# Kernel optimization log

Measured on AMD Instinct MI355X. Metric: run time of the kernel, lower is better.

The kernel has to match this reference:

```python
import jax, jax.numpy as jnp
import numpy as np


def setup_inputs() -> dict:
    key = jax.random.key(0)
    ks = jax.random.split(key, 6)
    bs, n_src, n_tgt = 4, 4096, 16384
    c_src, c_tgt = 256, 128
    xyz_target = jax.random.uniform(ks[0], (bs, n_tgt, 3), dtype=jnp.float32)
    xyz_source = jax.random.uniform(ks[1], (bs, n_src, 3), dtype=jnp.float32)
    feats_target = jax.random.normal(ks[2], (bs, n_tgt, c_tgt), dtype=jnp.float32)
    feats_source = jax.random.normal(ks[3], (bs, n_src, c_src), dtype=jnp.float32)
    # SharedMlP 1x1 conv weights (1,1,cin,cout) squeezed to (cin,cout)
    w1 = jax.random.normal(ks[4], (c_src + c_tgt, 256), dtype=jnp.float32) * (1.0 / np.sqrt(c_src + c_tgt))
    w2 = jax.random.normal(ks[5], (256, 256), dtype=jnp.float32) * (1.0 / np.sqrt(256))
    return {"xyz_target": xyz_target, "xyz_source": xyz_source,
            "feats_target": feats_target, "feats_source": feats_source,
            "w1": w1, "w2": w2}


def reference(xyz_target, xyz_source, feats_target, feats_source, w1, w2):
    # --- three_nn: full pairwise euclidean distance [bs, n_tgt, n_src] ---
    diff = xyz_target[:, :, None, :] - xyz_source[:, None, :, :]
    dis = jnp.linalg.norm(diff, axis=-1)                      # bs, n_tgt, n_src
    neg_dis, idx = jax.lax.top_k(-dis, 3)                     # 3 nearest
    nn_dis = jnp.maximum(-neg_dis, 1e-10)                     # bs, n_tgt, 3
    inv = 1.0 / nn_dis
    weight = inv / jnp.sum(inv, axis=-1, keepdims=True)       # bs, n_tgt, 3
    # --- three_interpolate: batched gather + weighted reduce ---
    feats_sel = jax.vmap(lambda f, i: f[i])(feats_source, idx)  # bs, n_tgt, 3, c
    w_sum = jnp.sum(weight, axis=-1, keepdims=True) + 1e-6
    interp = jnp.einsum('btk,btkc->btc', weight, feats_sel) / w_sum
    # --- concat skip features, 1x1-conv MLP (pointwise matmul) ---
    x = jnp.concatenate([interp, feats_target], axis=2)       # bs, n_tgt, 384
    x = jax.nn.relu(jnp.einsum('btc,cd->btd', x, w1))
    x = jax.nn.relu(jnp.einsum('btc,cd->btd', x, w2))
    return x
```

## Files before the change

### kernel.cpp

```cpp
#include <hip/hip_runtime.h>
#include <hip/hip_bf16.h>
#include <stdint.h>

#define BS 4
#define NS 4096
#define NT 16384
#define CT 128
#define NOUT 256
#define MTOT (BS*NT)
#define GR 8
#define NC (GR*GR*GR)
#define HCELL 0.125f

typedef __attribute__((ext_vector_type(4))) float floatx4;
typedef __attribute__((ext_vector_type(8))) unsigned short ushortx8;
typedef __attribute__((ext_vector_type(8))) __bf16 bf16x8;

__device__ __forceinline__ unsigned short f2bf(float f) {
  unsigned int u = __builtin_bit_cast(unsigned int, f);
  u += 0x7FFFu + ((u >> 16) & 1u);
  return (unsigned short)(u >> 16);
}
__device__ __forceinline__ float bf2f(unsigned short u) {
  return __builtin_bit_cast(float, ((unsigned int)u) << 16);
}
__device__ __forceinline__ int cell_of(float x) {
  int c = (int)(x * 8.0f);
  return min(7, max(0, c));
}
__device__ __forceinline__ bf16x8 ldb16(const unsigned short* p) {
  return __builtin_bit_cast(bf16x8, *(const ushortx8*)p);
}
__device__ __forceinline__ ushortx8 wsum8(ushortx8 a, ushortx8 c, ushortx8 e,
                                          float w0, float w1v, float w2v) {
  ushortx8 o;
  #pragma unroll
  for (int q = 0; q < 8; ++q)
    o[q] = f2bf(w0*bf2f(a[q]) + w1v*bf2f(c[q]) + w2v*bf2f(e[q]));
  return o;
}

__global__ __launch_bounds__(1024) void prep_kernel(
    const float* __restrict__ xyzs, const float* __restrict__ xyzt,
    const float* __restrict__ w1, const float* __restrict__ w2,
    float4* __restrict__ bsrc, int* __restrict__ soff, float4* __restrict__ stgt,
    unsigned short* __restrict__ w1at, unsigned short* __restrict__ w1bt,
    unsigned short* __restrict__ w2t) {
  int bid = blockIdx.x, tid = threadIdx.x;
  if (bid < 8) {
    __shared__ int cnt[NC];
    __shared__ int scan[NC];
    int b = bid & 3;
    bool isrc = bid < 4;
    int per = isrc ? (NS >> 10) : (NT >> 10);
    const float* in = isrc ? xyzs + (size_t)b * NS * 3 : xyzt + (size_t)b * NT * 3;
    float4* outp = isrc ? bsrc + (size_t)b * NS : stgt + (size_t)b * NT;
    if (tid < NC) cnt[tid] = 0;
    __syncthreads();
    for (int k = 0; k < per; ++k) {
      int p = k * 1024 + tid;
      float x = in[3*p], y = in[3*p+1], z = in[3*p+2];
      int c = (cell_of(z) * GR + cell_of(y)) * GR + cell_of(x);
      atomicAdd(&cnt[c], 1);
    }
    __syncthreads();
    if (tid < NC) scan[tid] = cnt[tid];
    __syncthreads();
    for (int off = 1; off < NC; off <<= 1) {
      int v = (tid < NC && tid >= off) ? scan[tid - off] : 0;
      __syncthreads();
      if (tid < NC) scan[tid] += v;
      __syncthreads();
    }
    if (tid < NC) {
      int excl = scan[tid] - cnt[tid];
      cnt[tid] = excl;
      if (isrc) soff[b * (NC + 1) + tid] = excl;
    }
    if (isrc && tid == 0) soff[b * (NC + 1) + NC] = NS;
    __syncthreads();
    for (int k = 0; k < per; ++k) {
      int p = k * 1024 + tid;
      float x = in[3*p], y = in[3*p+1], z = in[3*p+2];
      int c = (cell_of(z) * GR + cell_of(y)) * GR + cell_of(x);
      int slot = atomicAdd(&cnt[c], 1);
      outp[slot] = make_float4(x, y, z, __int_as_float(p));
    }
  } else {
    int i = (bid - 8) * 1024 + tid;
    int n = i >> 8, k = i & 255;
    w1at[i] = f2bf(w1[k * NOUT + n]);
    w2t[i]  = f2bf(w2[k * NOUT + n]);
    if (i < 256 * 128) {
      int n2 = i >> 7, k2 = i & 127;
      w1bt[i] = f2bf(w1[(256 + k2) * NOUT + n2]);
    }
  }
}

__device__ __forceinline__ void ins3(float sc, int jj,
    float& d0, float& d1, float& d2, int& i0, int& i1, int& i2) {
  bool l0 = sc < d0, l1 = sc < d1, l2 = sc < d2;
  d2 = l1 ? d1 : (l2 ? sc : d2);
  i2 = l1 ? i1 : (l2 ? jj : i2);
  d1 = l0 ? d0 : (l1 ? sc : d1);
  i1 = l0 ? i0 : (l1 ? jj : i1);
  d0 = l0 ? sc : d0;
  i0 = l0 ? jj : i0;
}

__device__ __forceinline__ void pair_merge(float& d0, float& d1, float& d2,
                                           int& i0, int& i1, int& i2,
                                           int delta, int sub) {
  float e0 = __shfl_xor(d0, delta);
  float e1 = __shfl_xor(d1, delta);
  float e2 = __shfl_xor(d2, delta);
  int   y0 = __shfl_xor(i0, delta);
  int   y1 = __shfl_xor(i1, delta);
  int   y2 = __shfl_xor(i2, delta);
  float a0,a1,a2,b0,b1,b2; int x0,x1,x2,z0,z1,z2;
  if ((sub & delta) == 0) { a0=d0;a1=d1;a2=d2; x0=i0;x1=i1;x2=i2;
                            b0=e0;b1=e1;b2=e2; z0=y0;z1=y1;z2=y2; }
  else                    { a0=e0;a1=e1;a2=e2; x0=y0;x1=y1;x2=y2;
                            b0=d0;b1=d1;b2=d2; z0=i0;z1=i1;z2=i2; }
  bool t = a0 <= b0;
  d0 = t ? a0 : b0; i0 = t ? x0 : z0;
  float na0 = t ? a1 : a0; int nx0 = t ? x1 : x0;
  float na1 = t ? a2 : a1; int nx1 = t ? x2 : x1;
  float nb0 = t ? b0 : b1; int nz0 = t ? z0 : z1;
  float nb1 = t ? b1 : b2; int nz1 = t ? z1 : z2;
  t = na0 <= nb0;
  d1 = t ? na0 : nb0; i1 = t ? nx0 : nz0;
  float ma0 = t ? na1 : na0; int mx0 = t ? nx1 : nx0;
  float mb0 = t ? nb0 : nb1; int mz0 = t ? nz0 : nz1;
  t = ma0 <= mb0;
  d2 = t ? ma0 : mb0; i2 = t ? mx0 : mz0;
}

__global__ __launch_bounds__(256) void nn_kernel(const float4* __restrict__ stgt,
    const float4* __restrict__ bsrc, const int* __restrict__ soff,
    int* __restrict__ idx_out, float* __restrict__ w_out) {
  __shared__ float4 s_src[NS];
  __shared__ int s_off[NC + 1];
  int tid = threadIdx.x;
  int b = blockIdx.x >> 7;
  int tseg = blockIdx.x & 127;
  for (int i = tid; i < NS; i += 256) s_src[i] = bsrc[(size_t)b * NS + i];
  for (int i = tid; i < NC + 1; i += 256) s_off[i] = soff[b * (NC + 1) + i];
  __syncthreads();
  int tpair = tid >> 1, half = tid & 1;
  float4 tg = stgt[(size_t)b * NT + tseg * 128 + tpair];
  float tx = tg.x, ty = tg.y, tz = tg.z;
  int cx = cell_of(tx), cy = cell_of(ty), cz = cell_of(tz);
  int wx = min(max(cx, 1), 6) - 1;
  int wy = min(max(cy, 1), 6) - 1;
  int wz = min(max(cz, 1), 6) - 1;
  float d0 = 1e30f, d1 = 1e30f, d2 = 1e30f;
  int i0 = 0, i1 = 0, i2 = 0;
  for (int r = half; r < 9; r += 2) {
    int ez = wz + r / 3, ey = wy + r % 3;
    int rowc = (ez * GR + ey) * GR + wx;
    int lo = s_off[rowc], hi = s_off[rowc + 3];
    for (int p = lo; p < hi; ++p) {
      float4 s = s_src[p];
      float dx = tx - s.x, dy = ty - s.y, dz = tz - s.z;
      float q = dx*dx + dy*dy + dz*dz;
      ins3(q, __float_as_int(s.w), d0, d1, d2, i0, i1, i2);
    }
  }
  pair_merge(d0, d1, d2, i0, i1, i2, 1, half);
  float clx = fminf(wx > 0 ? tx - wx * HCELL : 1e30f,
                    wx + 3 < GR ? (wx + 3) * HCELL - tx : 1e30f);
  float cly = fminf(wy > 0 ? ty - wy * HCELL : 1e30f,
                    wy + 3 < GR ? (wy + 3) * HCELL - ty : 1e30f);
  float clz = fminf(wz > 0 ? tz - wz * HCELL : 1e30f,
                    wz + 3 < GR ? (wz + 3) * HCELL - tz : 1e30f);
  float cl = fminf(clx, fminf(cly, clz));
  bool bad = d2 > cl * cl;
  if (__any(bad)) {
    if (bad) {
      d0 = d1 = d2 = 1e30f; i0 = i1 = i2 = 0;
      for (int p = half; p < NS; p += 2) {
        float4 s = s_src[p];
        float dx = tx - s.x, dy = ty - s.y, dz = tz - s.z;
        float q = dx*dx + dy*dy + dz*dz;
        ins3(q, __float_as_int(s.w), d0, d1, d2, i0, i1, i2);
      }
    }
    pair_merge(d0, d1, d2, i0, i1, i2, 1, half);
  }
  if (half == 0) {
    float r0 = fmaxf(sqrtf(d0), 1e-10f);
    float r1 = fmaxf(sqrtf(d1), 1e-10f);
    float r2 = fmaxf(sqrtf(d2), 1e-10f);
    float v0 = 1.f/r0, v1 = 1.f/r1, v2 = 1.f/r2;
    float sc = 1.f / ((v0 + v1 + v2) * (1.f + 1e-6f));
    size_t o = ((size_t)b * NT + tseg * 128 + tpair) * 3;
    idx_out[o] = i0; idx_out[o+1] = i1; idx_out[o+2] = i2;
    w_out[o] = v0*sc; w_out[o+1] = v1*sc; w_out[o+2] = v2*sc;
  }
}

__global__ __launch_bounds__(256, 4) void gemm_g(const float* __restrict__ fs,
    const unsigned short* __restrict__ w1at, unsigned short* __restrict__ G) {
  constexpr int LDT = 264;
  __shared__ __attribute__((aligned(16))) unsigned short sA[32 * LDT];
  int tid = threadIdx.x;
  int m0 = blockIdx.x * 32;
  int wave = tid >> 6, lane = tid & 63;
  int wn = wave * 64;
  int fr = lane & 15, quad = lane >> 4;
  const unsigned short* wbase = w1at + (size_t)(wn + fr) * 256 + quad * 8;
  #pragma unroll
  for (int i = 0; i < 4; ++i) {
    int u = tid + 256 * i;
    int r = u >> 5, k8 = (u & 31) * 8;
    const float* src = fs + (size_t)(m0 + r) * 256 + k8;
    float4 f0 = *(const float4*)src;
    float4 f1 = *(const float4*)(src + 4);
    ushortx8 o;
    o[0]=f2bf(f0.x); o[1]=f2bf(f0.y); o[2]=f2bf(f0.z); o[3]=f2bf(f0.w);
    o[4]=f2bf(f1.x); o[5]=f2bf(f1.y); o[6]=f2bf(f1.z); o[7]=f2bf(f1.w);
    *(ushortx8*)&sA[r * LDT + k8] = o;
  }
  __syncthreads();
  floatx4 zero = {0.f, 0.f, 0.f, 0.f};
  floatx4 acc[2][4];
  #pragma unroll
  for (int i = 0; i < 2; ++i)
    #pragma unroll
    for (int j = 0; j < 4; ++j) acc[i][j] = zero;
  bf16x8 wb[3][4];
  #pragma unroll
  for (int ni = 0; ni < 4; ++ni) wb[0][ni] = ldb16(wbase + (size_t)ni*16*256 + 0*32);
  #pragma unroll
  for (int ni = 0; ni < 4; ++ni) wb[1][ni] = ldb16(wbase + (size_t)ni*16*256 + 1*32);
  __builtin_amdgcn_sched_barrier(0);
  #pragma unroll
  for (int kt = 0; kt < 8; ++kt) {
    if (kt < 6) {
      #pragma unroll
      for (int ni = 0; ni < 4; ++ni)
        wb[(kt+2)%3][ni] = ldb16(wbase + (size_t)ni*16*256 + (kt+2)*32);
    }
    __builtin_amdgcn_sched_barrier(0);
    bf16x8 af[2];
    #pragma unroll
    for (int mi = 0; mi < 2; ++mi)
      af[mi] = ldb16(&sA[(mi*16 + fr)*LDT + kt*32 + quad*8]);
    #pragma unroll
    for (int mi = 0; mi < 2; ++mi)
      #pragma unroll
      for (int ni = 0; ni < 4; ++ni)
        acc[mi][ni] = __builtin_amdgcn_mfma_f32_16x16x32_bf16(
            af[mi], wb[kt%3][ni], acc[mi][ni], 0, 0, 0);
  }
  #pragma unroll
  for (int mi = 0; mi < 2; ++mi)
    #pragma unroll
    for (int ni = 0; ni < 4; ++ni)
      #pragma unroll
      for (int r = 0; r < 4; ++r) {
        int grow = m0 + mi*16 + quad*4 + r;
        int gcol = wn + ni*16 + fr;
        G[(size_t)grow * 256 + gcol] = f2bf(acc[mi][ni][r]);
      }
}

__global__ __launch_bounds__(512, 4) void fused_mlp(const float* __restrict__ ft,
    const unsigned short* __restrict__ G, const int* __restrict__ idxb,
    const float* __restrict__ wgtb, const float4* __restrict__ stgt,
    const unsigned short* __restrict__ w1bt, const unsigned short* __restrict__ w2t,
    float* __restrict__ out) {
  constexpr int LDI = 264;
  constexpr int LDF = 136;
  __shared__ __attribute__((aligned(16))) unsigned short sI[64 * LDI];
  __shared__ __attribute__((aligned(16))) unsigned short sF[64 * LDF];
  int tid = threadIdx.x;
  int row0 = blockIdx.x * 64;
  int b = row0 >> 14;
  const float4* st = stgt + ((size_t)b << 14) + (row0 & (NT - 1));
  const float* ftb = ft + (size_t)b * NT * CT;
  float* outb = out + (size_t)b * NT * NOUT;
  int wave = tid >> 6, lane = tid & 63;
  int wn = wave * 32;
  int fr = lane & 15, quad = lane >> 4;

  int r = tid >> 3, seg = tid & 7;
  const int* ip = idxb + (size_t)(row0 + r) * 3;
  const float* wp = wgtb + (size_t)(row0 + r) * 3;
  int g0i = ip[0], g1i = ip[1], g2i = ip[2];
  float w0 = wp[0], w1v = wp[1], w2v = wp[2];
  int rA = tid >> 4;
  int rB = rA + 32;
  int orig0 = __float_as_int(st[rA].w);
  int orig1 = __float_as_int(st[rB].w);

  bf16x8 wb1[2][4];
  #pragma unroll
  for (int ni = 0; ni < 2; ++ni)
    #pragma unroll
    for (int kt = 0; kt < 4; ++kt)
      wb1[ni][kt] = ldb16(w1bt + (size_t)(wn + ni*16 + fr) * CT + kt*32 + quad*8);
  __builtin_amdgcn_sched_barrier(0);

  const unsigned short* Gb = G + ((size_t)b << 20);
  const unsigned short* g0 = Gb + ((size_t)g0i << 8) + seg * 32;
  const unsigned short* g1 = Gb + ((size_t)g1i << 8) + seg * 32;
  const unsigned short* g2 = Gb + ((size_t)g2i << 8) + seg * 32;
  ushortx8 a0 = *(const ushortx8*)(g0 + 0);
  ushortx8 a1 = *(const ushortx8*)(g0 + 8);
  ushortx8 a2 = *(const ushortx8*)(g0 + 16);
  ushortx8 a3 = *(const ushortx8*)(g0 + 24);
  ushortx8 c0 = *(const ushortx8*)(g1 + 0);
  ushortx8 c1 = *(const ushortx8*)(g1 + 8);
  ushortx8 c2 = *(const ushortx8*)(g1 + 16);
  ushortx8 c3 = *(const ushortx8*)(g1 + 24);
  ushortx8 e0 = *(const ushortx8*)(g2 + 0);
  ushortx8 e1 = *(const ushortx8*)(g2 + 8);
  ushortx8 e2 = *(const ushortx8*)(g2 + 16);
  ushortx8 e3 = *(const ushortx8*)(g2 + 24);

  int k8 = (tid & 15) * 8;
  const float* srcA = ftb + (size_t)orig0 * CT + k8;
  const float* srcB = ftb + (size_t)orig1 * CT + k8;
  float4 fa0 = *(const float4*)srcA;
  float4 fa1 = *(const float4*)(srcA + 4);
  float4 fb0 = *(const float4*)srcB;
  float4 fb1 = *(const float4*)(srcB + 4);
  __builtin_amdgcn_sched_barrier(0);

  {
    unsigned short* dst = &sI[r * LDI + seg * 32];
    *(ushortx8*)(dst + 0)  = wsum8(a0, c0, e0, w0, w1v, w2v);
    *(ushortx8*)(dst + 8)  = wsum8(a1, c1, e1, w0, w1v, w2v);
    *(ushortx8*)(dst + 16) = wsum8(a2, c2, e2, w0, w1v, w2v);
    *(ushortx8*)(dst + 24) = wsum8(a3, c3, e3, w0, w1v, w2v);
  }
  {
    ushortx8 o;
    o[0]=f2bf(fa0.x); o[1]=f2bf(fa0.y); o[2]=f2bf(fa0.z); o[3]=f2bf(fa0.w);
    o[4]=f2bf(fa1.x); o[5]=f2bf(fa1.y); o[6]=f2bf(fa1.z); o[7]=f2bf(fa1.w);
    *(ushortx8*)&sF[rA * LDF + k8] = o;
    ushortx8 p;
    p[0]=f2bf(fb0.x); p[1]=f2bf(fb0.y); p[2]=f2bf(fb0.z); p[3]=f2bf(fb0.w);
    p[4]=f2bf(fb1.x); p[5]=f2bf(fb1.y); p[6]=f2bf(fb1.z); p[7]=f2bf(fb1.w);
    *(ushortx8*)&sF[rB * LDF + k8] = p;
  }
  __syncthreads();

  floatx4 zero = {0.f, 0.f, 0.f, 0.f};
  floatx4 acc[4][2];
  #pragma unroll
  for (int i = 0; i < 4; ++i)
    #pragma unroll
    for (int j = 0; j < 2; ++j) acc[i][j] = zero;

  #pragma unroll
  for (int kt = 0; kt < 4; ++kt) {
    bf16x8 af[4];
    #pragma unroll
    for (int mi = 0; mi < 4; ++mi)
      af[mi] = ldb16(&sF[(mi*16 + fr)*LDF + kt*32 + quad*8]);
    #pragma unroll
    for (int mi = 0; mi < 4; ++mi)
      #pragma unroll
      for (int ni = 0; ni < 2; ++ni)
        acc[mi][ni] = __builtin_amdgcn_mfma_f32_16x16x32_bf16(
            af[mi], wb1[ni][kt], acc[mi][ni], 0, 0, 0);
  }

  bf16x8 wb2[2][8];
  #pragma unroll
  for (int ni = 0; ni < 2; ++ni)
    #pragma unroll
    for (int kt = 0; kt < 8; ++kt)
      wb2[ni][kt] = ldb16(w2t + (size_t)(wn + ni*16 + fr) * NOUT + kt*32 + quad*8);
  __builtin_amdgcn_sched_barrier(0);

  #pragma unroll
  for (int mi = 0; mi < 4; ++mi)
    #pragma unroll
    for (int ni = 0; ni < 2; ++ni)
      #pragma unroll
      for (int rr = 0; rr < 4; ++rr) {
        int lr = mi*16 + quad*4 + rr;
        int lc = wn + ni*16 + fr;
        float v = acc[mi][ni][rr] + bf2f(sI[lr * LDI + lc]);
        sI[lr * LDI + lc] = f2bf(fmaxf(v, 0.f));
      }
  __syncthreads();

  #pragma unroll
  for (int i = 0; i < 4; ++i)
    #pragma unroll
    for (int j = 0; j < 2; ++j) acc[i][j] = zero;
  #pragma unroll
  for (int kt = 0; kt < 8; ++kt) {
    bf16x8 af[4];
    #pragma unroll
    for (int mi = 0; mi < 4; ++mi)
      af[mi] = ldb16(&sI[(mi*16 + fr)*LDI + kt*32 + quad*8]);
    #pragma unroll
    for (int mi = 0; mi < 4; ++mi)
      #pragma unroll
      for (int ni = 0; ni < 2; ++ni)
        acc[mi][ni] = __builtin_amdgcn_mfma_f32_16x16x32_bf16(
            af[mi], wb2[ni][kt], acc[mi][ni], 0, 0, 0);
  }
  #pragma unroll
  for (int mi = 0; mi < 4; ++mi)
    #pragma unroll
    for (int rr = 0; rr < 4; ++rr) {
      int lr = mi*16 + quad*4 + rr;
      int orig = __float_as_int(st[lr].w);
      float* orow = outb + (size_t)orig * NOUT;
      #pragma unroll
      for (int ni = 0; ni < 2; ++ni)
        orow[wn + ni*16 + fr] = fmaxf(acc[mi][ni][rr], 0.f);
    }
}

extern "C" void kernel_launch(void* const* d_in, const int* in_sizes, int n_in,
                              void* d_out, int out_size, void* d_ws, size_t ws_size,
                              hipStream_t stream) {
  (void)in_sizes; (void)n_in; (void)out_size; (void)ws_size;
  const float* xyzt = (const float*)d_in[0];
  const float* xyzs = (const float*)d_in[1];
  const float* ft   = (const float*)d_in[2];
  const float* fs   = (const float*)d_in[3];
  const float* w1   = (const float*)d_in[4];
  const float* w2   = (const float*)d_in[5];

  char* p = (char*)d_ws;
  unsigned short* w1at = (unsigned short*)p; p += (size_t)256*256*2;
  unsigned short* w1bt = (unsigned short*)p; p += (size_t)256*128*2;
  unsigned short* w2t  = (unsigned short*)p; p += (size_t)256*256*2;
  int*   idxb = (int*)p;   p += (size_t)MTOT*3*4;
  float* wgtb = (float*)p; p += (size_t)MTOT*3*4;
  unsigned short* G = (unsigned short*)p; p += (size_t)BS*NS*NOUT*2;
  float4* bsrc = (float4*)p; p += (size_t)BS*NS*16;
  float4* stgt = (float4*)p; p += (size_t)BS*NT*16;
  int*    soff = (int*)p;

  hipLaunchKernelGGL(prep_kernel, dim3(8 + 64), dim3(1024), 0, stream,
                     xyzs, xyzt, w1, w2, bsrc, soff, stgt, w1at, w1bt, w2t);
  hipLaunchKernelGGL(nn_kernel, dim3(512), dim3(256), 0, stream, stgt, bsrc, soff, idxb, wgtb);
  hipLaunchKernelGGL(gemm_g, dim3(BS*NS/32), dim3(256), 0, stream, fs, w1at, G);
  hipLaunchKernelGGL(fused_mlp, dim3(MTOT/64), dim3(512), 0, stream,
                     ft, G, idxb, wgtb, stgt, w1bt, w2t, (float*)d_out);
}
```

Before: 193.0 us.

## Drop precomputed source GEMM; interpolate raw features and run full K=384 GEMM

The separate gemm_g kernel, which projected source features through the first 256 rows of w1 before the gather, is removed. fused_mlp now gathers the three fp32 source feature rows, interpolates them into shared memory, and runs a single K=384 GEMM against a combined transposed w1. The weight fragments for both GEMMs are now streamed through a triple-buffered register prefetch instead of being preloaded in full. This removes one kernel launch and the bf16 G intermediate round trip, but gathers twice the bytes per neighbour (fp32 instead of bf16) and triples the first GEMM's K-work per target point (target points outnumber source points four to one).

After: 212.2 us. +10.0%, slower.

```diff
diff --git a/kernel.cpp b/kernel.cpp
--- a/kernel.cpp
+++ b/kernel.cpp
@@ -31,21 +31,12 @@
 __device__ __forceinline__ bf16x8 ldb16(const unsigned short* p) {
   return __builtin_bit_cast(bf16x8, *(const ushortx8*)p);
 }
-__device__ __forceinline__ ushortx8 wsum8(ushortx8 a, ushortx8 c, ushortx8 e,
-                                          float w0, float w1v, float w2v) {
-  ushortx8 o;
-  #pragma unroll
-  for (int q = 0; q < 8; ++q)
-    o[q] = f2bf(w0*bf2f(a[q]) + w1v*bf2f(c[q]) + w2v*bf2f(e[q]));
-  return o;
-}
 
 __global__ __launch_bounds__(1024) void prep_kernel(
     const float* __restrict__ xyzs, const float* __restrict__ xyzt,
     const float* __restrict__ w1, const float* __restrict__ w2,
     float4* __restrict__ bsrc, int* __restrict__ soff, float4* __restrict__ stgt,
-    unsigned short* __restrict__ w1at, unsigned short* __restrict__ w1bt,
-    unsigned short* __restrict__ w2t) {
+    unsigned short* __restrict__ w1t, unsigned short* __restrict__ w2t) {
   int bid = blockIdx.x, tid = threadIdx.x;
   if (bid < 8) {
     __shared__ int cnt[NC];
@@ -89,11 +80,15 @@
   } else {
     int i = (bid - 8) * 1024 + tid;
     int n = i >> 8, k = i & 255;
-    w1at[i] = f2bf(w1[k * NOUT + n]);
-    w2t[i]  = f2bf(w2[k * NOUT + n]);
-    if (i < 256 * 128) {
-      int n2 = i >> 7, k2 = i & 127;
-      w1bt[i] = f2bf(w1[(256 + k2) * NOUT + n2]);
+    w2t[i] = f2bf(w2[k * NOUT + n]);
+    {
+      int nn = i / 384, kk = i - nn * 384;
+      w1t[i] = f2bf(w1[kk * NOUT + nn]);
+    }
+    if (i < 32768) {
+      int j = 65536 + i;
+      int nn = j / 384, kk = j - nn * 384;
+      w1t[j] = f2bf(w1[kk * NOUT + nn]);
     }
   }
 }
@@ -201,86 +196,19 @@
   }
 }
 
-__global__ __launch_bounds__(256, 4) void gemm_g(const float* __restrict__ fs,
-    const unsigned short* __restrict__ w1at, unsigned short* __restrict__ G) {
-  constexpr int LDT = 264;
-  __shared__ __attribute__((aligned(16))) unsigned short sA[32 * LDT];
-  int tid = threadIdx.x;
-  int m0 = blockIdx.x * 32;
-  int wave = tid >> 6, lane = tid & 63;
-  int wn = wave * 64;
-  int fr = lane & 15, quad = lane >> 4;
-  const unsigned short* wbase = w1at + (size_t)(wn + fr) * 256 + quad * 8;
-  #pragma unroll
-  for (int i = 0; i < 4; ++i) {
-    int u = tid + 256 * i;
-    int r = u >> 5, k8 = (u & 31) * 8;
-    const float* src = fs + (size_t)(m0 + r) * 256 + k8;
-    float4 f0 = *(const float4*)src;
-    float4 f1 = *(const float4*)(src + 4);
-    ushortx8 o;
-    o[0]=f2bf(f0.x); o[1]=f2bf(f0.y); o[2]=f2bf(f0.z); o[3]=f2bf(f0.w);
-    o[4]=f2bf(f1.x); o[5]=f2bf(f1.y); o[6]=f2bf(f1.z); o[7]=f2bf(f1.w);
-    *(ushortx8*)&sA[r * LDT + k8] = o;
-  }
-  __syncthreads();
-  floatx4 zero = {0.f, 0.f, 0.f, 0.f};
-  floatx4 acc[2][4];
-  #pragma unroll
-  for (int i = 0; i < 2; ++i)
-    #pragma unroll
-    for (int j = 0; j < 4; ++j) acc[i][j] = zero;
-  bf16x8 wb[3][4];
-  #pragma unroll
-  for (int ni = 0; ni < 4; ++ni) wb[0][ni] = ldb16(wbase + (size_t)ni*16*256 + 0*32);
-  #pragma unroll
-  for (int ni = 0; ni < 4; ++ni) wb[1][ni] = ldb16(wbase + (size_t)ni*16*256 + 1*32);
-  __builtin_amdgcn_sched_barrier(0);
-  #pragma unroll
-  for (int kt = 0; kt < 8; ++kt) {
-    if (kt < 6) {
-      #pragma unroll
-      for (int ni = 0; ni < 4; ++ni)
-        wb[(kt+2)%3][ni] = ldb16(wbase + (size_t)ni*16*256 + (kt+2)*32);
-    }
-    __builtin_amdgcn_sched_barrier(0);
-    bf16x8 af[2];
-    #pragma unroll
-    for (int mi = 0; mi < 2; ++mi)
-      af[mi] = ldb16(&sA[(mi*16 + fr)*LDT + kt*32 + quad*8]);
-    #pragma unroll
-    for (int mi = 0; mi < 2; ++mi)
-      #pragma unroll
-      for (int ni = 0; ni < 4; ++ni)
-        acc[mi][ni] = __builtin_amdgcn_mfma_f32_16x16x32_bf16(
-            af[mi], wb[kt%3][ni], acc[mi][ni], 0, 0, 0);
-  }
-  #pragma unroll
-  for (int mi = 0; mi < 2; ++mi)
-    #pragma unroll
-    for (int ni = 0; ni < 4; ++ni)
-      #pragma unroll
-      for (int r = 0; r < 4; ++r) {
-        int grow = m0 + mi*16 + quad*4 + r;
-        int gcol = wn + ni*16 + fr;
-        G[(size_t)grow * 256 + gcol] = f2bf(acc[mi][ni][r]);
-      }
-}
-
 __global__ __launch_bounds__(512, 4) void fused_mlp(const float* __restrict__ ft,
-    const unsigned short* __restrict__ G, const int* __restrict__ idxb,
+    const float* __restrict__ fs, const int* __restrict__ idxb,
     const float* __restrict__ wgtb, const float4* __restrict__ stgt,
-    const unsigned short* __restrict__ w1bt, const unsigned short* __restrict__ w2t,
+    const unsigned short* __restrict__ w1t, const unsigned short* __restrict__ w2t,
     float* __restrict__ out) {
-  constexpr int LDI = 264;
-  constexpr int LDF = 136;
-  __shared__ __attribute__((aligned(16))) unsigned short sI[64 * LDI];
-  __shared__ __attribute__((aligned(16))) unsigned short sF[64 * LDF];
+  constexpr int LDA = 392;
+  __shared__ __attribute__((aligned(16))) unsigned short sA[64 * LDA];
   int tid = threadIdx.x;
   int row0 = blockIdx.x * 64;
   int b = row0 >> 14;
   const float4* st = stgt + ((size_t)b << 14) + (row0 & (NT - 1));
   const float* ftb = ft + (size_t)b * NT * CT;
+  const float* fsb = fs + (size_t)b * NS * 256;
   float* outb = out + (size_t)b * NT * NOUT;
   int wave = tid >> 6, lane = tid & 63;
   int wn = wave * 32;
@@ -296,31 +224,40 @@
   int orig0 = __float_as_int(st[rA].w);
   int orig1 = __float_as_int(st[rB].w);
 
-  bf16x8 wb1[2][4];
-  #pragma unroll
-  for (int ni = 0; ni < 2; ++ni)
-    #pragma unroll
-    for (int kt = 0; kt < 4; ++kt)
-      wb1[ni][kt] = ldb16(w1bt + (size_t)(wn + ni*16 + fr) * CT + kt*32 + quad*8);
+  const float* p0 = fsb + (size_t)g0i * 256 + seg * 32;
+  const float* p1 = fsb + (size_t)g1i * 256 + seg * 32;
+  const float* p2 = fsb + (size_t)g2i * 256 + seg * 32;
+  float4 xa[3][4], xb[3][4];
+  #pragma unroll
+  for (int j = 0; j < 4; ++j) {
+    xa[0][j] = ((const float4*)p0)[j];
+    xa[1][j] = ((const float4*)p1)[j];
+    xa[2][j] = ((const float4*)p2)[j];
+  }
+  #pragma unroll
+  for (int j = 0; j < 4; ++j) {
+    xb[0][j] = ((const float4*)(p0 + 16))[j];
+    xb[1][j] = ((const float4*)(p1 + 16))[j];
+    xb[2][j] = ((const float4*)(p2 + 16))[j];
+  }
   __builtin_amdgcn_sched_barrier(0);
 
-  const unsigned short* Gb = G + ((size_t)b << 20);
-  const unsigned short* g0 = Gb + ((size_t)g0i << 8) + seg * 32;
-  const unsigned short* g1 = Gb + ((size_t)g1i << 8) + seg * 32;
-  const unsigned short* g2 = Gb + ((size_t)g2i << 8) + seg * 32;
-  ushortx8 a0 = *(const ushortx8*)(g0 + 0);
-  ushortx8 a1 = *(const ushortx8*)(g0 + 8);
-  ushortx8 a2 = *(const ushortx8*)(g0 + 16);
-  ushortx8 a3 = *(const ushortx8*)(g0 + 24);
-  ushortx8 c0 = *(const ushortx8*)(g1 + 0);
-  ushortx8 c1 = *(const ushortx8*)(g1 + 8);
-  ushortx8 c2 = *(const ushortx8*)(g1 + 16);
-  ushortx8 c3 = *(const ushortx8*)(g1 + 24);
-  ushortx8 e0 = *(const ushortx8*)(g2 + 0);
-  ushortx8 e1 = *(const ushortx8*)(g2 + 8);
-  ushortx8 e2 = *(const ushortx8*)(g2 + 16);
-  ushortx8 e3 = *(const ushortx8*)(g2 + 24);
-
+  {
+    unsigned short* dst = &sA[r * LDA + seg * 32];
+    #pragma unroll
+    for (int h = 0; h < 2; ++h) {
+      ushortx8 o;
+      #pragma unroll
+      for (int q = 0; q < 8; ++q) {
+        int e = h * 8 + q;
+        float v = w0 * xa[0][e >> 2][e & 3]
+                + w1v * xa[1][e >> 2][e & 3]
+                + w2v * xa[2][e >> 2][e & 3];
+        o[q] = f2bf(v);
+      }
+      *(ushortx8*)(dst + h * 8) = o;
+    }
+  }
   int k8 = (tid & 15) * 8;
   const float* srcA = ftb + (size_t)orig0 * CT + k8;
   const float* srcB = ftb + (size_t)orig1 * CT + k8;
@@ -331,22 +268,39 @@
   __builtin_amdgcn_sched_barrier(0);
 
   {
-    unsigned short* dst = &sI[r * LDI + seg * 32];
-    *(ushortx8*)(dst + 0)  = wsum8(a0, c0, e0, w0, w1v, w2v);
-    *(ushortx8*)(dst + 8)  = wsum8(a1, c1, e1, w0, w1v, w2v);
-    *(ushortx8*)(dst + 16) = wsum8(a2, c2, e2, w0, w1v, w2v);
-    *(ushortx8*)(dst + 24) = wsum8(a3, c3, e3, w0, w1v, w2v);
+    unsigned short* dst = &sA[r * LDA + seg * 32 + 16];
+    #pragma unroll
+    for (int h = 0; h < 2; ++h) {
+      ushortx8 o;
+      #pragma unroll
+      for (int q = 0; q < 8; ++q) {
+        int e = h * 8 + q;
+        float v = w0 * xb[0][e >> 2][e & 3]
+                + w1v * xb[1][e >> 2][e & 3]
+                + w2v * xb[2][e >> 2][e & 3];
+        o[q] = f2bf(v);
+      }
+      *(ushortx8*)(dst + h * 8) = o;
+    }
   }
   {
     ushortx8 o;
     o[0]=f2bf(fa0.x); o[1]=f2bf(fa0.y); o[2]=f2bf(fa0.z); o[3]=f2bf(fa0.w);
     o[4]=f2bf(fa1.x); o[5]=f2bf(fa1.y); o[6]=f2bf(fa1.z); o[7]=f2bf(fa1.w);
-    *(ushortx8*)&sF[rA * LDF + k8] = o;
+    *(ushortx8*)&sA[rA * LDA + 256 + k8] = o;
     ushortx8 p;
     p[0]=f2bf(fb0.x); p[1]=f2bf(fb0.y); p[2]=f2bf(fb0.z); p[3]=f2bf(fb0.w);
     p[4]=f2bf(fb1.x); p[5]=f2bf(fb1.y); p[6]=f2bf(fb1.z); p[7]=f2bf(fb1.w);
-    *(ushortx8*)&sF[rB * LDF + k8] = p;
-  }
+    *(ushortx8*)&sA[rB * LDA + 256 + k8] = p;
+  }
+
+  const unsigned short* wb1base = w1t + (size_t)(wn + fr) * 384 + quad * 8;
+  bf16x8 w1r[3][2];
+  #pragma unroll
+  for (int ni = 0; ni < 2; ++ni) w1r[0][ni] = ldb16(wb1base + (size_t)ni*16*384 + 0*32);
+  #pragma unroll
+  for (int ni = 0; ni < 2; ++ni) w1r[1][ni] = ldb16(wb1base + (size_t)ni*16*384 + 1*32);
+  __builtin_amdgcn_sched_barrier(0);
   __syncthreads();
 
   floatx4 zero = {0.f, 0.f, 0.f, 0.f};
@@ -357,27 +311,34 @@
     for (int j = 0; j < 2; ++j) acc[i][j] = zero;
 
   #pragma unroll
-  for (int kt = 0; kt < 4; ++kt) {
+  for (int kt = 0; kt < 12; ++kt) {
+    if (kt < 10) {
+      #pragma unroll
+      for (int ni = 0; ni < 2; ++ni)
+        w1r[(kt+2)%3][ni] = ldb16(wb1base + (size_t)ni*16*384 + (kt+2)*32);
+    }
+    __builtin_amdgcn_sched_barrier(0);
     bf16x8 af[4];
     #pragma unroll
     for (int mi = 0; mi < 4; ++mi)
-      af[mi] = ldb16(&sF[(mi*16 + fr)*LDF + kt*32 + quad*8]);
+      af[mi] = ldb16(&sA[(mi*16 + fr)*LDA + kt*32 + quad*8]);
     #pragma unroll
     for (int mi = 0; mi < 4; ++mi)
       #pragma unroll
       for (int ni = 0; ni < 2; ++ni)
         acc[mi][ni] = __builtin_amdgcn_mfma_f32_16x16x32_bf16(
-            af[mi], wb1[ni][kt], acc[mi][ni], 0, 0, 0);
-  }
-
-  bf16x8 wb2[2][8];
-  #pragma unroll
-  for (int ni = 0; ni < 2; ++ni)
-    #pragma unroll
-    for (int kt = 0; kt < 8; ++kt)
-      wb2[ni][kt] = ldb16(w2t + (size_t)(wn + ni*16 + fr) * NOUT + kt*32 + quad*8);
+            af[mi], w1r[kt%3][ni], acc[mi][ni], 0, 0, 0);
+  }
+
+  const unsigned short* wb2base = w2t + (size_t)(wn + fr) * 256 + quad * 8;
+  bf16x8 w2r[3][2];
+  #pragma unroll
+  for (int ni = 0; ni < 2; ++ni) w2r[0][ni] = ldb16(wb2base + (size_t)ni*16*256 + 0*32);
+  #pragma unroll
+  for (int ni = 0; ni < 2; ++ni) w2r[1][ni] = ldb16(wb2base + (size_t)ni*16*256 + 1*32);
   __builtin_amdgcn_sched_barrier(0);
 
+  __syncthreads();
   #pragma unroll
   for (int mi = 0; mi < 4; ++mi)
     #pragma unroll
@@ -386,8 +347,7 @@
       for (int rr = 0; rr < 4; ++rr) {
         int lr = mi*16 + quad*4 + rr;
         int lc = wn + ni*16 + fr;
-        float v = acc[mi][ni][rr] + bf2f(sI[lr * LDI + lc]);
-        sI[lr * LDI + lc] = f2bf(fmaxf(v, 0.f));
+        sA[lr * LDA + lc] = f2bf(fmaxf(acc[mi][ni][rr], 0.f));
       }
   __syncthreads();
 
@@ -397,16 +357,22 @@
     for (int j = 0; j < 2; ++j) acc[i][j] = zero;
   #pragma unroll
   for (int kt = 0; kt < 8; ++kt) {
+    if (kt < 6) {
+      #pragma unroll
+      for (int ni = 0; ni < 2; ++ni)
+        w2r[(kt+2)%3][ni] = ldb16(wb2base + (size_t)ni*16*256 + (kt+2)*32);
+    }
+    __builtin_amdgcn_sched_barrier(0);
     bf16x8 af[4];
     #pragma unroll
     for (int mi = 0; mi < 4; ++mi)
-      af[mi] = ldb16(&sI[(mi*16 + fr)*LDI + kt*32 + quad*8]);
+      af[mi] = ldb16(&sA[(mi*16 + fr)*LDA + kt*32 + quad*8]);
     #pragma unroll
     for (int mi = 0; mi < 4; ++mi)
       #pragma unroll
       for (int ni = 0; ni < 2; ++ni)
         acc[mi][ni] = __builtin_amdgcn_mfma_f32_16x16x32_bf16(
-            af[mi], wb2[ni][kt], acc[mi][ni], 0, 0, 0);
+            af[mi], w2r[kt%3][ni], acc[mi][ni], 0, 0, 0);
   }
   #pragma unroll
   for (int mi = 0; mi < 4; ++mi)
@@ -433,20 +399,17 @@
   const float* w2   = (const float*)d_in[5];
 
   char* p = (char*)d_ws;
-  unsigned short* w1at = (unsigned short*)p; p += (size_t)256*256*2;
-  unsigned short* w1bt = (unsigned short*)p; p += (size_t)256*128*2;
-  unsigned short* w2t  = (unsigned short*)p; p += (size_t)256*256*2;
+  unsigned short* w1t = (unsigned short*)p; p += (size_t)256*384*2;
+  unsigned short* w2t = (unsigned short*)p; p += (size_t)256*256*2;
   int*   idxb = (int*)p;   p += (size_t)MTOT*3*4;
   float* wgtb = (float*)p; p += (size_t)MTOT*3*4;
-  unsigned short* G = (unsigned short*)p; p += (size_t)BS*NS*NOUT*2;
   float4* bsrc = (float4*)p; p += (size_t)BS*NS*16;
   float4* stgt = (float4*)p; p += (size_t)BS*NT*16;
   int*    soff = (int*)p;
 
   hipLaunchKernelGGL(prep_kernel, dim3(8 + 64), dim3(1024), 0, stream,
-                     xyzs, xyzt, w1, w2, bsrc, soff, stgt, w1at, w1bt, w2t);
+                     xyzs, xyzt, w1, w2, bsrc, soff, stgt, w1t, w2t);
   hipLaunchKernelGGL(nn_kernel, dim3(512), dim3(256), 0, stream, stgt, bsrc, soff, idxb, wgtb);
-  hipLaunchKernelGGL(gemm_g, dim3(BS*NS/32), dim3(256), 0, stream, fs, w1at, G);
   hipLaunchKernelGGL(fused_mlp, dim3(MTOT/64), dim3(512), 0, stream,
-                     ft, G, idxb, wgtb, stgt, w1bt, w2t, (float*)d_out);
-}
+                     ft, fs, idxb, wgtb, stgt, w1t, w2t, (float*)d_out);
+}
```

## Queue fallback brute-force queries in shared memory and process each with a full wave

Applied to the files above, without the earlier changes.

Targets whose 3x3x3 cell window search cannot guarantee correctness are now appended to a shared-memory queue instead of being brute-forced by a thread pair. After a block barrier, each wave takes one queued query and scans all 4096 sources across its 64 lanes, then reduces with a butterfly merge. This removes divergence, where a whole wave stalled on a full 2048-point scan for a few bad lanes. The cost is an extra __syncthreads, a shared atomic, and a butterfly reduction per queued query.

Measured after the change: 192.4 us. Within noise of the previous version (-0.3%).

```diff
diff --git a/kernel.cpp b/kernel.cpp
--- a/kernel.cpp
+++ b/kernel.cpp
@@ -142,9 +142,12 @@
     int* __restrict__ idx_out, float* __restrict__ w_out) {
   __shared__ float4 s_src[NS];
   __shared__ int s_off[NC + 1];
+  __shared__ float4 s_badq[128];
+  __shared__ int s_badn;
   int tid = threadIdx.x;
   int b = blockIdx.x >> 7;
   int tseg = blockIdx.x & 127;
+  if (tid == 0) s_badn = 0;
   for (int i = tid; i < NS; i += 256) s_src[i] = bsrc[(size_t)b * NS + i];
   for (int i = tid; i < NC + 1; i += 256) s_off[i] = soff[b * (NC + 1) + i];
   __syncthreads();
@@ -177,27 +180,48 @@
                     wz + 3 < GR ? (wz + 3) * HCELL - tz : 1e30f);
   float cl = fminf(clx, fminf(cly, clz));
   bool bad = d2 > cl * cl;
-  if (__any(bad)) {
+  if (half == 0) {
     if (bad) {
-      d0 = d1 = d2 = 1e30f; i0 = i1 = i2 = 0;
-      for (int p = half; p < NS; p += 2) {
-        float4 s = s_src[p];
-        float dx = tx - s.x, dy = ty - s.y, dz = tz - s.z;
-        float q = dx*dx + dy*dy + dz*dz;
-        ins3(q, __float_as_int(s.w), d0, d1, d2, i0, i1, i2);
-      }
-    }
-    pair_merge(d0, d1, d2, i0, i1, i2, 1, half);
-  }
-  if (half == 0) {
-    float r0 = fmaxf(sqrtf(d0), 1e-10f);
-    float r1 = fmaxf(sqrtf(d1), 1e-10f);
-    float r2 = fmaxf(sqrtf(d2), 1e-10f);
-    float v0 = 1.f/r0, v1 = 1.f/r1, v2 = 1.f/r2;
-    float sc = 1.f / ((v0 + v1 + v2) * (1.f + 1e-6f));
-    size_t o = ((size_t)b * NT + tseg * 128 + tpair) * 3;
-    idx_out[o] = i0; idx_out[o+1] = i1; idx_out[o+2] = i2;
-    w_out[o] = v0*sc; w_out[o+1] = v1*sc; w_out[o+2] = v2*sc;
+      int slot = atomicAdd(&s_badn, 1);
+      s_badq[slot] = make_float4(tx, ty, tz, __int_as_float(tseg * 128 + tpair));
+    } else {
+      float r0 = fmaxf(sqrtf(d0), 1e-10f);
+      float r1 = fmaxf(sqrtf(d1), 1e-10f);
+      float r2 = fmaxf(sqrtf(d2), 1e-10f);
+      float v0 = 1.f/r0, v1 = 1.f/r1, v2 = 1.f/r2;
+      float sc = 1.f / ((v0 + v1 + v2) * (1.f + 1e-6f));
+      size_t o = ((size_t)b * NT + tseg * 128 + tpair) * 3;
+      idx_out[o] = i0; idx_out[o+1] = i1; idx_out[o+2] = i2;
+      w_out[o] = v0*sc; w_out[o+1] = v1*sc; w_out[o+2] = v2*sc;
+    }
+  }
+  __syncthreads();
+  int nbad = s_badn;
+  int wv = tid >> 6, ln = tid & 63;
+  for (int e = wv; e < nbad; e += 4) {
+    float4 tq = s_badq[e];
+    float qx = tq.x, qy = tq.y, qz = tq.z;
+    float f0 = 1e30f, f1 = 1e30f, f2 = 1e30f;
+    int   j0 = 0, j1 = 0, j2 = 0;
+    for (int p = ln; p < NS; p += 64) {
+      float4 s = s_src[p];
+      float dx = qx - s.x, dy = qy - s.y, dz = qz - s.z;
+      float q = dx*dx + dy*dy + dz*dz;
+      ins3(q, __float_as_int(s.w), f0, f1, f2, j0, j1, j2);
+    }
+    #pragma unroll
+    for (int delta = 1; delta <= 32; delta <<= 1)
+      pair_merge(f0, f1, f2, j0, j1, j2, delta, ln);
+    if (ln == 0) {
+      float r0 = fmaxf(sqrtf(f0), 1e-10f);
+      float r1 = fmaxf(sqrtf(f1), 1e-10f);
+      float r2 = fmaxf(sqrtf(f2), 1e-10f);
+      float v0 = 1.f/r0, v1 = 1.f/r1, v2 = 1.f/r2;
+      float sc = 1.f / ((v0 + v1 + v2) * (1.f + 1e-6f));
+      size_t o = ((size_t)b * NT + __float_as_int(tq.w)) * 3;
+      idx_out[o] = j0; idx_out[o+1] = j1; idx_out[o+2] = j2;
+      w_out[o] = v0*sc; w_out[o+1] = v1*sc; w_out[o+2] = v2*sc;
+    }
   }
 }
 
```
